# Kernel optimization log

Hardware: AMD Instinct MI355X
Metric: run time of the kernel (lower is better)

Reference implementation:

```python
import jax, jax.numpy as jnp
import numpy as np

EMBED = 1024
HEADS = 16
HEAD_DIM = EMBED // HEADS


def setup_inputs() -> dict:
    key = jax.random.key(0)
    ks = jax.random.split(key, 12)
    N, S, E = 4, 2048, EMBED
    scale = 1.0 / np.sqrt(E)
    inp = {
        "values": jax.random.normal(ks[0], (N, S, E), dtype=jnp.float32),
        "keys": jax.random.normal(ks[1], (N, S, E), dtype=jnp.float32),
        "query": jax.random.normal(ks[2], (N, S, E), dtype=jnp.float32),
        "mask": jnp.ones((N, 1, 1, S), dtype=jnp.int32),
        # Linear params: y = x @ W + b (W stored as [in, out])
        "Wv": jax.random.normal(ks[3], (E, E), dtype=jnp.float32) * scale,
        "bv": jnp.zeros((E,), dtype=jnp.float32),
        "Wk": jax.random.normal(ks[4], (E, E), dtype=jnp.float32) * scale,
        "bk": jnp.zeros((E,), dtype=jnp.float32),
        "Wq": jax.random.normal(ks[5], (E, E), dtype=jnp.float32) * scale,
        "bq": jnp.zeros((E,), dtype=jnp.float32),
        "Wo": jax.random.normal(ks[6], (E, E), dtype=jnp.float32) * scale,
        "bo": jnp.zeros((E,), dtype=jnp.float32),
    }
    return inp


def reference(values, keys, query, mask, Wv, bv, Wk, bk, Wq, bq, Wo, bo):
    N, Q, E = query.shape
    V = values.shape[1]
    K = keys.shape[1]
    v = (values @ Wv + bv).reshape(N, V, HEADS, HEAD_DIM)
    k = (keys @ Wk + bk).reshape(N, K, HEADS, HEAD_DIM)
    q = (query @ Wq + bq).reshape(N, Q, HEADS, HEAD_DIM)
    # energy: [N, H, Q, K]
    energy = jnp.einsum("nqhd,nkhd->nhqk", q, k)
    energy = jnp.where(mask == 0, jnp.float32(-1e20), energy)
    # NOTE: original scales by sqrt(embed_size), not sqrt(head_dim)
    attn = jax.nn.softmax(energy / jnp.sqrt(jnp.float32(E)), axis=3)
    out = jnp.einsum("nhql,nlhd->nqhd", attn, v).reshape(N, Q, E)
    return out @ Wo + bo
```

## Files before the change

### kernel.cpp

```cpp
#include <hip/hip_runtime.h>

#define H 16
#define DH 64
#define S 2048
#define E 1024
#define NB 4

typedef short short8_t __attribute__((ext_vector_type(8)));
typedef float float4_t __attribute__((ext_vector_type(4)));

__device__ inline unsigned short f2bf(float f) {
    union { float f; unsigned u; } v; v.f = f;
    unsigned r = v.u + 0x7fffu + ((v.u >> 16) & 1u);
    return (unsigned short)(r >> 16);
}

__device__ __forceinline__ unsigned pk_bf16(float a, float b) {
    union { float f; unsigned u; } ua, ub;
    ua.f = a; ub.f = b;
    unsigned ra = ua.u + 0x7fffu + ((ua.u >> 16) & 1u);
    unsigned rb = ub.u + 0x7fffu + ((ub.u >> 16) & 1u);
    return __builtin_amdgcn_perm(rb, ra, 0x07060302u);
}

__device__ __forceinline__ void async_copy16(const unsigned short* g, unsigned short* l) {
    __builtin_amdgcn_global_load_lds(
        (const __attribute__((address_space(1))) unsigned int*)g,
        (__attribute__((address_space(3))) unsigned int*)l, 16, 0, 0);
}

__global__ __launch_bounds__(256) void xcvt_kernel(
    const float* __restrict__ v, const float* __restrict__ k,
    const float* __restrict__ q, unsigned short* __restrict__ xv,
    unsigned short* __restrict__ xk, unsigned short* __restrict__ xq)
{
    const int z = blockIdx.y;
    const float* src = (z == 0) ? v : (z == 1) ? k : q;
    unsigned short* dst = (z == 0) ? xv : (z == 1) ? xk : xq;
    size_t i0 = ((size_t)blockIdx.x * 256 + threadIdx.x) * 8;
    float4 f0 = *reinterpret_cast<const float4*>(src + i0);
    float4 f1 = *reinterpret_cast<const float4*>(src + i0 + 4);
    uint4 o;
    o.x = pk_bf16(f0.x, f0.y); o.y = pk_bf16(f0.z, f0.w);
    o.z = pk_bf16(f1.x, f1.y); o.w = pk_bf16(f1.z, f1.w);
    *reinterpret_cast<uint4*>(dst + i0) = o;
}

__global__ __launch_bounds__(256) void wcvt_kernel(
    const float* __restrict__ Wv, const float* __restrict__ Wk,
    const float* __restrict__ Wq, const float* __restrict__ Wo,
    unsigned short* __restrict__ Wt)
{
    __shared__ float tile[64][65];
    const float* W = (blockIdx.z == 0) ? Wv : (blockIdx.z == 1) ? Wk
                   : (blockIdx.z == 2) ? Wq : Wo;
    unsigned short* out = Wt + (size_t)blockIdx.z * (E * E);
    const int k0 = blockIdx.x * 64, n0 = blockIdx.y * 64;
    const int tid = threadIdx.x;
#pragma unroll
    for (int i = 0; i < 4; ++i) {
        int c = i * 256 + tid;
        int kl = c >> 4, nl4 = (c & 15) * 4;
        float4 v = *reinterpret_cast<const float4*>(W + (size_t)(k0 + kl) * E + n0 + nl4);
        tile[kl][nl4 + 0] = v.x; tile[kl][nl4 + 1] = v.y;
        tile[kl][nl4 + 2] = v.z; tile[kl][nl4 + 3] = v.w;
    }
    __syncthreads();
#pragma unroll
    for (int i = 0; i < 4; ++i) {
        int c = i * 256 + tid;
        int nl = c >> 4, kl4 = (c & 15) * 4;
        ushort4 o;
        o.x = f2bf(tile[kl4 + 0][nl]); o.y = f2bf(tile[kl4 + 1][nl]);
        o.z = f2bf(tile[kl4 + 2][nl]); o.w = f2bf(tile[kl4 + 3][nl]);
        *reinterpret_cast<ushort4*>(out + (size_t)(n0 + nl) * E + k0 + kl4) = o;
    }
}

__global__ __launch_bounds__(256) void proj_kernel(
    const unsigned short* __restrict__ A, const unsigned short* __restrict__ WT,
    const float* __restrict__ bias, unsigned short* __restrict__ out, int mode)
{
    __shared__ __align__(16) unsigned short As[128][64];
    __shared__ __align__(16) unsigned short Bs[128][64];

    const int tid = threadIdx.x;
    const int m0 = blockIdx.y * 128;
    const int n0 = blockIdx.x * 128;
    const int wave = tid >> 6, lane = tid & 63;
    const int wm = wave >> 1, wn = wave & 1;
    const int quad = lane >> 4, l16 = lane & 15;
    const int r8 = lane >> 3;
    const int c8 = (lane & 7) ^ (r8 & 7);

    float4_t acc[4][4];
#pragma unroll
    for (int i = 0; i < 4; ++i)
#pragma unroll
        for (int j = 0; j < 4; ++j) { float4_t z = {0.f,0.f,0.f,0.f}; acc[i][j] = z; }

    for (int k0 = 0; k0 < E; k0 += 64) {
#pragma unroll
        for (int j = 0; j < 4; ++j) {
            int row = wave * 32 + j * 8 + r8;
            async_copy16(A  + (size_t)(m0 + row) * E + k0 + c8 * 8, &As[wave * 32 + j * 8][0]);
            async_copy16(WT + (size_t)(n0 + row) * E + k0 + c8 * 8, &Bs[wave * 32 + j * 8][0]);
        }
        __syncthreads();
#pragma unroll
        for (int kk = 0; kk < 2; ++kk) {
            short8_t a[4], b[4];
#pragma unroll
            for (int mi = 0; mi < 4; ++mi)
                a[mi] = *reinterpret_cast<const short8_t*>(
                    &As[wm * 64 + mi * 16 + l16][((kk * 4 + quad) ^ (l16 & 7)) * 8]);
#pragma unroll
            for (int nj = 0; nj < 4; ++nj)
                b[nj] = *reinterpret_cast<const short8_t*>(
                    &Bs[wn * 64 + nj * 16 + l16][((kk * 4 + quad) ^ (l16 & 7)) * 8]);
#pragma unroll
            for (int mi = 0; mi < 4; ++mi)
#pragma unroll
                for (int nj = 0; nj < 4; ++nj)
                    acc[mi][nj] = __builtin_amdgcn_mfma_f32_16x16x32_bf16(a[mi], b[nj], acc[mi][nj], 0, 0, 0);
        }
        __syncthreads();
    }
#pragma unroll
    for (int mi = 0; mi < 4; ++mi) {
#pragma unroll
        for (int nj = 0; nj < 4; ++nj) {
            int gcol = n0 + wn * 64 + nj * 16 + l16;
            float bvv = bias[gcol];
            int h = gcol >> 6, d = gcol & 63;
#pragma unroll
            for (int r = 0; r < 4; ++r) {
                int gm = m0 + wm * 64 + mi * 16 + quad * 4 + r;
                float val = acc[mi][nj][r] + bvv;
                int n = gm >> 11, s = gm & 2047;
                size_t addr;
                if (mode == 0)
                    addr = (((size_t)(n * H + h)) * DH + d) * S + s;
                else
                    addr = (((size_t)(n * H + h)) * S + s) * DH + d;
                out[addr] = f2bf(val);
            }
        }
    }
}

__global__ __launch_bounds__(256) void flash_kernel(
    const unsigned short* __restrict__ Qb, const unsigned short* __restrict__ Kb,
    const unsigned short* __restrict__ VTb, const int* __restrict__ mask,
    unsigned short* __restrict__ AO)
{
    __shared__ __align__(16) unsigned short Ks[2][64][64];
    __shared__ __align__(16) unsigned short Vs[2][64][64];
    __shared__ __align__(16) unsigned short Ps[4][32][72];
    __shared__ float am[2][64];
    __shared__ float lbuf[4][32];

    const int tid = threadIdx.x;
    const int wave = tid >> 6, lane = tid & 63;
    const int quad = lane >> 4, l16 = lane & 15;
    const int r8 = lane >> 3;
    const int c8 = (lane & 7) ^ (r8 & 7);
    const int qt = blockIdx.x;
    const int nh = blockIdx.y;
    const int n = nh >> 4, h = nh & 15;
    const size_t hb = (size_t)nh * S * DH;
    const unsigned short* Qh = Qb + hb;
    const unsigned short* Kh = Kb + hb;
    const unsigned short* Vh = VTb + hb;
    const int* mp = mask + n * S;

    const float c1 = 0.03125f * 1.4426950408889634f;
    const float C2_UNMASK = -23.083120654223414f;
    const float C2_MASK   = -1.44e20f;

    short8_t qa[2][2];
#pragma unroll
    for (int qb2 = 0; qb2 < 2; ++qb2)
#pragma unroll
        for (int kk = 0; kk < 2; ++kk) {
            int row = qt * 128 + wave * 32 + qb2 * 16 + l16;
            qa[qb2][kk] = *reinterpret_cast<const short8_t*>(Qh + (size_t)row * DH + kk * 32 + quad * 8);
        }

    float4_t o[2][4];
#pragma unroll
    for (int mi = 0; mi < 2; ++mi)
#pragma unroll
        for (int nj = 0; nj < 4; ++nj) { float4_t z = {0.f,0.f,0.f,0.f}; o[mi][nj] = z; }
    float lsum[2] = {0.f, 0.f};

#pragma unroll
    for (int j = 0; j < 2; ++j) {
        int row = wave * 16 + j * 8 + r8;
        async_copy16(Kh + (size_t)row * DH + c8 * 8, &Ks[0][wave * 16 + j * 8][0]);
        async_copy16(Vh + (size_t)row * S + c8 * 8,  &Vs[0][wave * 16 + j * 8][0]);
    }
    if (tid < 64) am[0][tid] = (mp[tid] == 0) ? C2_MASK : C2_UNMASK;

    for (int it = 0; it < 32; ++it) {
        const int cur = it & 1, nxt = cur ^ 1;
        __syncthreads();

        const int kn = (it < 31) ? (it + 1) * 64 : 0;
#pragma unroll
        for (int j = 0; j < 2; ++j) {
            int row = wave * 16 + j * 8 + r8;
            async_copy16(Kh + (size_t)(kn + row) * DH + c8 * 8, &Ks[nxt][wave * 16 + j * 8][0]);
            async_copy16(Vh + (size_t)row * S + kn + c8 * 8,    &Vs[nxt][wave * 16 + j * 8][0]);
        }
        if (tid < 64) am[nxt][tid] = (mp[kn + tid] == 0) ? C2_MASK : C2_UNMASK;

        float4_t st[4][2];
#pragma unroll
        for (int kvb = 0; kvb < 4; ++kvb)
#pragma unroll
            for (int qb2 = 0; qb2 < 2; ++qb2) { float4_t z = {0.f,0.f,0.f,0.f}; st[kvb][qb2] = z; }
#pragma unroll
        for (int kk = 0; kk < 2; ++kk) {
            short8_t ak[4];
#pragma unroll
            for (int kvb = 0; kvb < 4; ++kvb)
                ak[kvb] = *reinterpret_cast<const short8_t*>(
                    &Ks[cur][kvb * 16 + l16][((kk * 4 + quad) ^ (l16 & 7)) * 8]);
#pragma unroll
            for (int kvb = 0; kvb < 4; ++kvb)
#pragma unroll
                for (int qb2 = 0; qb2 < 2; ++qb2)
                    st[kvb][qb2] = __builtin_amdgcn_mfma_f32_16x16x32_bf16(ak[kvb], qa[qb2][kk], st[kvb][qb2], 0, 0, 0);
        }

#pragma unroll
        for (int kvb = 0; kvb < 4; ++kvb) {
            float4 c2v = *reinterpret_cast<const float4*>(&am[cur][kvb * 16 + quad * 4]);
#pragma unroll
            for (int qb2 = 0; qb2 < 2; ++qb2) {
                float p0 = __builtin_amdgcn_exp2f(st[kvb][qb2][0] * c1 + c2v.x);
                float p1 = __builtin_amdgcn_exp2f(st[kvb][qb2][1] * c1 + c2v.y);
                float p2 = __builtin_amdgcn_exp2f(st[kvb][qb2][2] * c1 + c2v.z);
                float p3 = __builtin_amdgcn_exp2f(st[kvb][qb2][3] * c1 + c2v.w);
                lsum[qb2] += (p0 + p1) + (p2 + p3);
                unsigned w0 = pk_bf16(p0, p1);
                unsigned w1 = pk_bf16(p2, p3);
                *reinterpret_cast<uint2*>(&Ps[wave][qb2 * 16 + l16][kvb * 16 + quad * 4]) =
                    make_uint2(w0, w1);
            }
        }

#pragma unroll
        for (int kk = 0; kk < 2; ++kk) {
            short8_t pa[2], vb[4];
#pragma unroll
            for (int mi = 0; mi < 2; ++mi)
                pa[mi] = *reinterpret_cast<const short8_t*>(&Ps[wave][mi * 16 + l16][kk * 32 + quad * 8]);
#pragma unroll
            for (int nj = 0; nj < 4; ++nj)
                vb[nj] = *reinterpret_cast<const short8_t*>(
                    &Vs[cur][nj * 16 + l16][((kk * 4 + quad) ^ (l16 & 7)) * 8]);
#pragma unroll
            for (int mi = 0; mi < 2; ++mi)
#pragma unroll
                for (int nj = 0; nj < 4; ++nj)
                    o[mi][nj] = __builtin_amdgcn_mfma_f32_16x16x32_bf16(pa[mi], vb[nj], o[mi][nj], 0, 0, 0);
        }
    }

    lsum[0] += __shfl_xor(lsum[0], 16); lsum[0] += __shfl_xor(lsum[0], 32);
    lsum[1] += __shfl_xor(lsum[1], 16); lsum[1] += __shfl_xor(lsum[1], 32);
    if (lane < 16) { lbuf[wave][lane] = lsum[0]; lbuf[wave][16 + lane] = lsum[1]; }

#pragma unroll
    for (int mi = 0; mi < 2; ++mi) {
        float4 lv = *reinterpret_cast<const float4*>(&lbuf[wave][mi * 16 + quad * 4]);
#pragma unroll
        for (int r = 0; r < 4; ++r) {
            float invl = __builtin_amdgcn_rcpf(((const float*)&lv)[r]);
            int qrow = qt * 128 + wave * 32 + mi * 16 + quad * 4 + r;
            size_t gm = (size_t)n * S + qrow;
#pragma unroll
            for (int nj = 0; nj < 4; ++nj) {
                int col = h * DH + nj * 16 + l16;
                AO[gm * E + col] = f2bf(o[mi][nj][r] * invl);
            }
        }
    }
}

__global__ __launch_bounds__(256) void ogemm_kernel(
    const unsigned short* __restrict__ A, const unsigned short* __restrict__ WT,
    const float* __restrict__ bias, float* __restrict__ out)
{
    __shared__ __align__(16) unsigned short As[128][64];
    __shared__ __align__(16) unsigned short Bs[128][64];

    const int tid = threadIdx.x;
    const int m0 = blockIdx.y * 128;
    const int n0 = blockIdx.x * 128;
    const int wave = tid >> 6, lane = tid & 63;
    const int wm = wave >> 1, wn = wave & 1;
    const int quad = lane >> 4, l16 = lane & 15;
    const int r8 = lane >> 3;
    const int c8 = (lane & 7) ^ (r8 & 7);

    float4_t acc[4][4];
#pragma unroll
    for (int i = 0; i < 4; ++i)
#pragma unroll
        for (int j = 0; j < 4; ++j) { float4_t z = {0.f,0.f,0.f,0.f}; acc[i][j] = z; }

    for (int k0 = 0; k0 < E; k0 += 64) {
#pragma unroll
        for (int j = 0; j < 4; ++j) {
            int row = wave * 32 + j * 8 + r8;
            async_copy16(A  + (size_t)(m0 + row) * E + k0 + c8 * 8, &As[wave * 32 + j * 8][0]);
            async_copy16(WT + (size_t)(n0 + row) * E + k0 + c8 * 8, &Bs[wave * 32 + j * 8][0]);
        }
        __syncthreads();
#pragma unroll
        for (int kk = 0; kk < 2; ++kk) {
            short8_t a[4], b[4];
#pragma unroll
            for (int mi = 0; mi < 4; ++mi)
                a[mi] = *reinterpret_cast<const short8_t*>(
                    &As[wm * 64 + mi * 16 + l16][((kk * 4 + quad) ^ (l16 & 7)) * 8]);
#pragma unroll
            for (int nj = 0; nj < 4; ++nj)
                b[nj] = *reinterpret_cast<const short8_t*>(
                    &Bs[wn * 64 + nj * 16 + l16][((kk * 4 + quad) ^ (l16 & 7)) * 8]);
#pragma unroll
            for (int mi = 0; mi < 4; ++mi)
#pragma unroll
                for (int nj = 0; nj < 4; ++nj)
                    acc[mi][nj] = __builtin_amdgcn_mfma_f32_16x16x32_bf16(a[mi], b[nj], acc[mi][nj], 0, 0, 0);
        }
        __syncthreads();
    }
#pragma unroll
    for (int mi = 0; mi < 4; ++mi)
#pragma unroll
        for (int nj = 0; nj < 4; ++nj) {
            int gcol = n0 + wn * 64 + nj * 16 + l16;
            float bvv = bias[gcol];
#pragma unroll
            for (int r = 0; r < 4; ++r) {
                int gm = m0 + wm * 64 + mi * 16 + quad * 4 + r;
                out[(size_t)gm * E + gcol] = acc[mi][nj][r] + bvv;
            }
        }
}

extern "C" void kernel_launch(void* const* d_in, const int* in_sizes, int n_in,
                              void* d_out, int out_size, void* d_ws, size_t ws_size,
                              hipStream_t stream) {
    const float* values = (const float*)d_in[0];
    const float* keys   = (const float*)d_in[1];
    const float* query  = (const float*)d_in[2];
    const int*   mask   = (const int*)d_in[3];
    const float* Wv = (const float*)d_in[4];  const float* bv = (const float*)d_in[5];
    const float* Wk = (const float*)d_in[6];  const float* bk = (const float*)d_in[7];
    const float* Wq = (const float*)d_in[8];  const float* bq = (const float*)d_in[9];
    const float* Wo = (const float*)d_in[10]; const float* bo = (const float*)d_in[11];
    float* out = (float*)d_out;

    char* ws = (char*)d_ws;
    unsigned short* Wt = (unsigned short*)ws;
    unsigned short* xv = (unsigned short*)(ws + 8388608);
    unsigned short* xk = (unsigned short*)(ws + 25165824);
    unsigned short* xq = (unsigned short*)(ws + 41943040);
    unsigned short* vt = (unsigned short*)(ws + 58720256);
    unsigned short* kb = xv;
    unsigned short* qb = xk;
    unsigned short* ao = xq;

    xcvt_kernel<<<dim3(4096, 3), 256, 0, stream>>>(values, keys, query, xv, xk, xq);
    wcvt_kernel<<<dim3(16, 16, 4), 256, 0, stream>>>(Wv, Wk, Wq, Wo, Wt);
    proj_kernel<<<dim3(8, 64), 256, 0, stream>>>(xv, Wt,           bv, vt, 0);
    proj_kernel<<<dim3(8, 64), 256, 0, stream>>>(xk, Wt + 1048576, bk, kb, 1);
    proj_kernel<<<dim3(8, 64), 256, 0, stream>>>(xq, Wt + 2097152, bq, qb, 1);
    flash_kernel<<<dim3(16, 64), 256, 0, stream>>>(qb, kb, vt, mask, ao);
    ogemm_kernel<<<dim3(8, 64), 256, 0, stream>>>(ao, Wt + 3145728, bo, out);
}
```

Measured before the change: 405.1 us.

## Double-buffer LDS tiles in projection and output GEMM kernels

Both the QKV projection GEMM and the output GEMM now hold two LDS buffers each for A and B tiles. The next k-slice is prefetched with async copies while MFMAs run on the current slice, and one of the two barriers per iteration is dropped. The aim is to hide global-to-LDS load latency behind matrix math. In exchange, LDS use per block doubles to 64KB, which can lower the number of resident blocks per CU.

After: 394.9 us. 2.5% less time.

```diff
diff --git a/kernel.cpp b/kernel.cpp
--- a/kernel.cpp
+++ b/kernel.cpp
@@ -81,8 +81,8 @@
     const unsigned short* __restrict__ A, const unsigned short* __restrict__ WT,
     const float* __restrict__ bias, unsigned short* __restrict__ out, int mode)
 {
-    __shared__ __align__(16) unsigned short As[128][64];
-    __shared__ __align__(16) unsigned short Bs[128][64];
+    __shared__ __align__(16) unsigned short As[2][128][64];
+    __shared__ __align__(16) unsigned short Bs[2][128][64];
 
     const int tid = threadIdx.x;
     const int m0 = blockIdx.y * 128;
@@ -99,32 +99,43 @@
 #pragma unroll
         for (int j = 0; j < 4; ++j) { float4_t z = {0.f,0.f,0.f,0.f}; acc[i][j] = z; }
 
-    for (int k0 = 0; k0 < E; k0 += 64) {
-#pragma unroll
-        for (int j = 0; j < 4; ++j) {
-            int row = wave * 32 + j * 8 + r8;
-            async_copy16(A  + (size_t)(m0 + row) * E + k0 + c8 * 8, &As[wave * 32 + j * 8][0]);
-            async_copy16(WT + (size_t)(n0 + row) * E + k0 + c8 * 8, &Bs[wave * 32 + j * 8][0]);
-        }
+#pragma unroll
+    for (int j = 0; j < 4; ++j) {
+        int row = wave * 32 + j * 8 + r8;
+        async_copy16(A  + (size_t)(m0 + row) * E + c8 * 8, &As[0][wave * 32 + j * 8][0]);
+        async_copy16(WT + (size_t)(n0 + row) * E + c8 * 8, &Bs[0][wave * 32 + j * 8][0]);
+    }
+
+    for (int it = 0; it < 16; ++it) {
+        const int cur = it & 1, nxt = cur ^ 1;
         __syncthreads();
+
+        if (it < 15) {
+            const int kn = (it + 1) * 64;
+#pragma unroll
+            for (int j = 0; j < 4; ++j) {
+                int row = wave * 32 + j * 8 + r8;
+                async_copy16(A  + (size_t)(m0 + row) * E + kn + c8 * 8, &As[nxt][wave * 32 + j * 8][0]);
+                async_copy16(WT + (size_t)(n0 + row) * E + kn + c8 * 8, &Bs[nxt][wave * 32 + j * 8][0]);
+            }
+        }
 #pragma unroll
         for (int kk = 0; kk < 2; ++kk) {
             short8_t a[4], b[4];
 #pragma unroll
             for (int mi = 0; mi < 4; ++mi)
                 a[mi] = *reinterpret_cast<const short8_t*>(
-                    &As[wm * 64 + mi * 16 + l16][((kk * 4 + quad) ^ (l16 & 7)) * 8]);
+                    &As[cur][wm * 64 + mi * 16 + l16][((kk * 4 + quad) ^ (l16 & 7)) * 8]);
 #pragma unroll
             for (int nj = 0; nj < 4; ++nj)
                 b[nj] = *reinterpret_cast<const short8_t*>(
-                    &Bs[wn * 64 + nj * 16 + l16][((kk * 4 + quad) ^ (l16 & 7)) * 8]);
+                    &Bs[cur][wn * 64 + nj * 16 + l16][((kk * 4 + quad) ^ (l16 & 7)) * 8]);
 #pragma unroll
             for (int mi = 0; mi < 4; ++mi)
 #pragma unroll
                 for (int nj = 0; nj < 4; ++nj)
                     acc[mi][nj] = __builtin_amdgcn_mfma_f32_16x16x32_bf16(a[mi], b[nj], acc[mi][nj], 0, 0, 0);
         }
-        __syncthreads();
     }
 #pragma unroll
     for (int mi = 0; mi < 4; ++mi) {
@@ -294,8 +305,8 @@
     const unsigned short* __restrict__ A, const unsigned short* __restrict__ WT,
     const float* __restrict__ bias, float* __restrict__ out)
 {
-    __shared__ __align__(16) unsigned short As[128][64];
-    __shared__ __align__(16) unsigned short Bs[128][64];
+    __shared__ __align__(16) unsigned short As[2][128][64];
+    __shared__ __align__(16) unsigned short Bs[2][128][64];
 
     const int tid = threadIdx.x;
     const int m0 = blockIdx.y * 128;
@@ -312,32 +323,43 @@
 #pragma unroll
         for (int j = 0; j < 4; ++j) { float4_t z = {0.f,0.f,0.f,0.f}; acc[i][j] = z; }
 
-    for (int k0 = 0; k0 < E; k0 += 64) {
-#pragma unroll
-        for (int j = 0; j < 4; ++j) {
-            int row = wave * 32 + j * 8 + r8;
-            async_copy16(A  + (size_t)(m0 + row) * E + k0 + c8 * 8, &As[wave * 32 + j * 8][0]);
-            async_copy16(WT + (size_t)(n0 + row) * E + k0 + c8 * 8, &Bs[wave * 32 + j * 8][0]);
-        }
+#pragma unroll
+    for (int j = 0; j < 4; ++j) {
+        int row = wave * 32 + j * 8 + r8;
+        async_copy16(A  + (size_t)(m0 + row) * E + c8 * 8, &As[0][wave * 32 + j * 8][0]);
+        async_copy16(WT + (size_t)(n0 + row) * E + c8 * 8, &Bs[0][wave * 32 + j * 8][0]);
+    }
+
+    for (int it = 0; it < 16; ++it) {
+        const int cur = it & 1, nxt = cur ^ 1;
         __syncthreads();
+
+        if (it < 15) {
+            const int kn = (it + 1) * 64;
+#pragma unroll
+            for (int j = 0; j < 4; ++j) {
+                int row = wave * 32 + j * 8 + r8;
+                async_copy16(A  + (size_t)(m0 + row) * E + kn + c8 * 8, &As[nxt][wave * 32 + j * 8][0]);
+                async_copy16(WT + (size_t)(n0 + row) * E + kn + c8 * 8, &Bs[nxt][wave * 32 + j * 8][0]);
+            }
+        }
 #pragma unroll
         for (int kk = 0; kk < 2; ++kk) {
             short8_t a[4], b[4];
 #pragma unroll
             for (int mi = 0; mi < 4; ++mi)
                 a[mi] = *reinterpret_cast<const short8_t*>(
-                    &As[wm * 64 + mi * 16 + l16][((kk * 4 + quad) ^ (l16 & 7)) * 8]);
+                    &As[cur][wm * 64 + mi * 16 + l16][((kk * 4 + quad) ^ (l16 & 7)) * 8]);
 #pragma unroll
             for (int nj = 0; nj < 4; ++nj)
                 b[nj] = *reinterpret_cast<const short8_t*>(
-                    &Bs[wn * 64 + nj * 16 + l16][((kk * 4 + quad) ^ (l16 & 7)) * 8]);
+                    &Bs[cur][wn * 64 + nj * 16 + l16][((kk * 4 + quad) ^ (l16 & 7)) * 8]);
 #pragma unroll
             for (int mi = 0; mi < 4; ++mi)
 #pragma unroll
                 for (int nj = 0; nj < 4; ++nj)
                     acc[mi][nj] = __builtin_amdgcn_mfma_f32_16x16x32_bf16(a[mi], b[nj], acc[mi][nj], 0, 0, 0);
         }
-        __syncthreads();
     }
 #pragma unroll
     for (int mi = 0; mi < 4; ++mi)
```
